# Kernel tuning notes

Measured on AMD Instinct MI355X. Metric: run time of the kernel, lower is better.

Reference implementation:

```python
import jax, jax.numpy as jnp
import numpy as np

N_NODES = 10000
N_EDGES = 160000
NUM_REL = 16
NUM_BLOCKS = 32
BLOCK_SIZE = 4  # input_dim 128 = 32 * 4
INPUT_DIM = NUM_BLOCKS * BLOCK_SIZE


def setup_inputs() -> dict:
    key = jax.random.key(0)
    ks = jax.random.split(key, 6)
    std = float(np.sqrt(2.0) / (2 * BLOCK_SIZE))  # matches reset_parameters
    return {
        "x": jax.random.normal(ks[0], (N_NODES, INPUT_DIM), dtype=jnp.float32),
        "node_keep_mask": jnp.ones((N_NODES,), dtype=bool),
        "source": jax.random.randint(ks[1], (N_EDGES,), 0, N_NODES),
        "target": jax.random.randint(ks[2], (N_EDGES,), 0, N_NODES),
        "edge_type": jax.random.randint(ks[3], (N_EDGES,), 0, NUM_REL),
        "edge_weights": jax.random.uniform(ks[4], (N_EDGES,), dtype=jnp.float32),
        "blocks": jax.random.normal(ks[5], (NUM_REL + 1, NUM_BLOCKS, BLOCK_SIZE, BLOCK_SIZE), dtype=jnp.float32) * std,
    }


def reference(x, node_keep_mask, source, target, edge_type, edge_weights, blocks):
    n = x.shape[0]
    _, nb, bs, _ = blocks.shape
    xb = x.reshape(n, nb, bs)  # (N, B, bs)
    # self-loop transform with last block set; dropped-out nodes stay zero
    self_msg = jnp.einsum('nbi,bij->nbj', xb, blocks[-1])
    out = jnp.where(node_keep_mask[:, None, None], self_msg, 0.0)
    # symmetrize edges: messages flow both directions with same relation/weight
    src2 = jnp.concatenate([source, target])
    tgt2 = jnp.concatenate([target, source])
    et2 = jnp.concatenate([edge_type, edge_type])
    ew2 = jnp.concatenate([edge_weights, edge_weights])
    # per-edge block-diagonal matmul: gather relation blocks then 4x4 block GEMMs
    w_e = blocks[et2]                              # (2E, B, bs, bs)
    m = jnp.einsum('ebi,ebij->ebj', xb[src2], w_e)  # (2E, B, bs)
    m = m * ew2[:, None, None]
    out = out + jax.ops.segment_sum(m, tgt2, num_segments=n)
    return out.reshape(n, nb * bs)
```

## Files before the change

### kernel.cpp

```cpp
#include <hip/hip_runtime.h>

#define INPUT_DIM 128
#define NB 32
#define BS 4
#define CAP 128
#define WSTRIDE_U 12
#define GBLOCKS 1250

typedef _Float16 h2 __attribute__((ext_vector_type(2)));
union HU { unsigned int u; h2 h; };

__device__ inline unsigned int pack_f16(float a, float b) {
    HU v; v.h = h2{(_Float16)a, (_Float16)b}; return v.u;
}
__device__ inline h2 as_h2(unsigned int u) { HU v; v.u = u; return v.h; }

__device__ inline float dot2(h2 a, h2 b, float c) {
    return __builtin_amdgcn_fdot2(a, b, c, false);
}


__global__ void prep_kernel(const float* __restrict__ x, unsigned int* __restrict__ xh,
                            const int* __restrict__ src, const int* __restrict__ tgt,
                            const int* __restrict__ etype, const float* __restrict__ ew,
                            int* __restrict__ counts, int2* __restrict__ msg,
                            int n_edges, int nx8) {
    int i = blockIdx.x * blockDim.x + threadIdx.x;
    if (i < nx8) {
        const float4 a = *(const float4*)(x + (size_t)i * 8);
        const float4 b = *(const float4*)(x + (size_t)i * 8 + 4);
        uint4 o;
        o.x = pack_f16(a.x, a.y);
        o.y = pack_f16(a.z, a.w);
        o.z = pack_f16(b.x, b.y);
        o.w = pack_f16(b.z, b.w);
        *(uint4*)(xh + (size_t)i * 4) = o;
    }
    if (i < n_edges) {
        int s = src[i], t = tgt[i];
        int pk_base = etype[i] << 16;
        int wbits = __float_as_int(ew[i]);
        int pf = atomicAdd(&counts[t], 1);
        msg[t * CAP + pf] = make_int2(s | pk_base, wbits);
        int pb = atomicAdd(&counts[s], 1);
        msg[s * CAP + pb] = make_int2(t | pk_base, wbits);
    }
}

__global__ __launch_bounds__(256, 6)
void gather_kernel(const float* __restrict__ x,
                   const unsigned int* __restrict__ xh,
                   const int* __restrict__ keep,
                   const float* __restrict__ blocks,
                   const int* __restrict__ counts,
                   const int2* __restrict__ msg,
                   float* __restrict__ out, int n_nodes) {
    __shared__ unsigned int Wlds[16 * NB * WSTRIDE_U];

    for (int bi = threadIdx.x; bi < 16 * NB; bi += 256) {
        const float4 r0 = ((const float4*)blocks)[bi * 4 + 0];
        const float4 r1 = ((const float4*)blocks)[bi * 4 + 1];
        const float4 r2 = ((const float4*)blocks)[bi * 4 + 2];
        const float4 r3 = ((const float4*)blocks)[bi * 4 + 3];
        uint4 q0, q1;
        q0.x = pack_f16(r0.x, r1.x); q0.y = pack_f16(r2.x, r3.x);
        q0.z = pack_f16(r0.y, r1.y); q0.w = pack_f16(r2.y, r3.y);
        q1.x = pack_f16(r0.z, r1.z); q1.y = pack_f16(r2.z, r3.z);
        q1.z = pack_f16(r0.w, r1.w); q1.w = pack_f16(r2.w, r3.w);
        *(uint4*)&Wlds[bi * WSTRIDE_U + 0] = q0;
        *(uint4*)&Wlds[bi * WSTRIDE_U + 4] = q1;
    }
    __syncthreads();

    int lane = threadIdx.x & 63;
    int b = lane & 31;
    int slot = lane >> 5;
    int wave_id = (blockIdx.x * blockDim.x + threadIdx.x) >> 6;
    int n_waves = gridDim.x * (blockDim.x >> 6);

    #define DO_MSG(PK, W)                                                     \
        {                                                                     \
            int s_ = (PK) & 0xFFFF;                                           \
            int r_ = (PK) >> 16;                                              \
            const unsigned int* Wp_ = &Wlds[(r_ * NB + b) * WSTRIDE_U];       \
            const uint4 q0 = *(const uint4*)(Wp_ + 0);                        \
            const uint4 q1 = *(const uint4*)(Wp_ + 4);                        \
            const uint2 xp = *(const uint2*)(xh + s_ * 64 + 2 * b);           \
            const h2 xl = as_h2(xp.x), xhh = as_h2(xp.y);                     \
            float m0 = dot2(xl, as_h2(q0.x), dot2(xhh, as_h2(q0.y), 0.f));    \
            float m1 = dot2(xl, as_h2(q0.z), dot2(xhh, as_h2(q0.w), 0.f));    \
            float m2 = dot2(xl, as_h2(q1.x), dot2(xhh, as_h2(q1.y), 0.f));    \
            float m3 = dot2(xl, as_h2(q1.z), dot2(xhh, as_h2(q1.w), 0.f));    \
            acc.x += (W) * m0;                                                \
            acc.y += (W) * m1;                                                \
            acc.z += (W) * m2;                                                \
            acc.w += (W) * m3;                                                \
        }

    for (int n = wave_id; n < n_nodes; n += n_waves) {
        float4 acc = make_float4(0.f, 0.f, 0.f, 0.f);

        if (slot == 0 && keep[n] != 0) {
            const float4 xv = *(const float4*)(x + (size_t)n * INPUT_DIM + b * BS);
            const float* Wp = blocks + (((size_t)16 * NB + b) << 4);
            const float4 c0 = *(const float4*)(Wp + 0);
            const float4 c1 = *(const float4*)(Wp + 4);
            const float4 c2 = *(const float4*)(Wp + 8);
            const float4 c3 = *(const float4*)(Wp + 12);
            acc.x = xv.x * c0.x + xv.y * c1.x + xv.z * c2.x + xv.w * c3.x;
            acc.y = xv.x * c0.y + xv.y * c1.y + xv.z * c2.y + xv.w * c3.y;
            acc.z = xv.x * c0.z + xv.y * c1.z + xv.z * c2.z + xv.w * c3.z;
            acc.w = xv.x * c0.w + xv.y * c1.w + xv.z * c2.w + xv.w * c3.w;
        }

        int cnt = counts[n];
        int base = n * CAP;
        int p = 0;
        for (; p + 8 <= cnt; p += 8) {
            int2 m0 = msg[base + p + 0 + slot];
            int2 m1 = msg[base + p + 2 + slot];
            int2 m2 = msg[base + p + 4 + slot];
            int2 m3 = msg[base + p + 6 + slot];
            float w0 = __int_as_float(m0.y);
            float w1 = __int_as_float(m1.y);
            float w2 = __int_as_float(m2.y);
            float w3 = __int_as_float(m3.y);
            DO_MSG(m0.x, w0);
            DO_MSG(m1.x, w1);
            DO_MSG(m2.x, w2);
            DO_MSG(m3.x, w3);
        }
        for (; p < cnt; p += 2) {
            if (p + slot < cnt) {
                int2 m = msg[base + p + slot];
                DO_MSG(m.x, __int_as_float(m.y));
            }
        }

        acc.x += __shfl_xor(acc.x, 32, 64);
        acc.y += __shfl_xor(acc.y, 32, 64);
        acc.z += __shfl_xor(acc.z, 32, 64);
        acc.w += __shfl_xor(acc.w, 32, 64);

        if (slot == 0)
            *(float4*)(out + (size_t)n * INPUT_DIM + b * BS) = acc;
    }
    #undef DO_MSG
}

extern "C" void kernel_launch(void* const* d_in, const int* in_sizes, int n_in,
                              void* d_out, int out_size, void* d_ws, size_t ws_size,
                              hipStream_t stream) {
    const float* x       = (const float*)d_in[0];
    const int* km        = (const int*)d_in[1];
    const int* source    = (const int*)d_in[2];
    const int* target    = (const int*)d_in[3];
    const int* edge_type = (const int*)d_in[4];
    const float* edge_w  = (const float*)d_in[5];
    const float* blocks  = (const float*)d_in[6];
    float* out           = (float*)d_out;

    int n_nodes = in_sizes[0] / INPUT_DIM;
    int n_edges = in_sizes[2];
    int nx8     = n_nodes * INPUT_DIM / 8;

    int* counts      = (int*)d_ws;
    unsigned int* xh = (unsigned int*)((char*)d_ws + 65536);
    int2* msg        = (int2*)((char*)d_ws + 65536 + (size_t)n_nodes * INPUT_DIM * 2);

    hipMemsetAsync(counts, 0, n_nodes * sizeof(int), stream);
    int prep_threads = (n_edges > nx8) ? n_edges : nx8;
    prep_kernel<<<(prep_threads + 255) / 256, 256, 0, stream>>>(
        x, xh, source, target, edge_type, edge_w, counts, msg, n_edges, nx8);
    gather_kernel<<<GBLOCKS, 256, 0, stream>>>(
        x, xh, km, blocks, counts, msg, out, n_nodes);
}
```

Baseline: 117.0 us.

## Precompute per-relation transformed node features and gather them per edge

The prep kernel now computes x·W_r for every node and all 17 relation block sets, storing the results as fp16 in a large Y table. The gather kernel then only loads one precomputed row per message and accumulates it scaled by the edge weight, replacing the per-edge LDS weight load and dot products. This trades per-edge compute (320k messages) for a dense transform over 17×10000 nodes and a 17-fold larger gather table (~43 MB), which spreads the random gathers over more memory and lowers cache locality. The gather grid is also resized to one wave per node, and prep_threads now covers n_nodes*NB rather than the max of edges and nx8.

```diff
diff --git a/kernel.cpp b/kernel.cpp
--- a/kernel.cpp
+++ b/kernel.cpp
@@ -4,8 +4,7 @@
 #define NB 32
 #define BS 4
 #define CAP 128
-#define WSTRIDE_U 12
-#define GBLOCKS 1250
+#define NREL 17
 
 typedef _Float16 h2 __attribute__((ext_vector_type(2)));
 union HU { unsigned int u; h2 h; };
@@ -15,27 +14,40 @@
 }
 __device__ inline h2 as_h2(unsigned int u) { HU v; v.u = u; return v.h; }
 
-__device__ inline float dot2(h2 a, h2 b, float c) {
-    return __builtin_amdgcn_fdot2(a, b, c, false);
-}
 
+__global__ __launch_bounds__(256)
+void prep_kernel(const float* __restrict__ x, const float* __restrict__ blocks,
+                 const int* __restrict__ src, const int* __restrict__ tgt,
+                 const int* __restrict__ etype, const float* __restrict__ ew,
+                 int* __restrict__ counts, int2* __restrict__ msg,
+                 unsigned int* __restrict__ Y, int n_edges, int n_nodes) {
+    __shared__ float Wlds[NREL * NB * 16];
 
-__global__ void prep_kernel(const float* __restrict__ x, unsigned int* __restrict__ xh,
-                            const int* __restrict__ src, const int* __restrict__ tgt,
-                            const int* __restrict__ etype, const float* __restrict__ ew,
-                            int* __restrict__ counts, int2* __restrict__ msg,
-                            int n_edges, int nx8) {
+    for (int i = threadIdx.x; i < NREL * NB * 4; i += 256)
+        ((float4*)Wlds)[i] = ((const float4*)blocks)[i];
+    __syncthreads();
+
     int i = blockIdx.x * blockDim.x + threadIdx.x;
-    if (i < nx8) {
-        const float4 a = *(const float4*)(x + (size_t)i * 8);
-        const float4 b = *(const float4*)(x + (size_t)i * 8 + 4);
-        uint4 o;
-        o.x = pack_f16(a.x, a.y);
-        o.y = pack_f16(a.z, a.w);
-        o.z = pack_f16(b.x, b.y);
-        o.w = pack_f16(b.z, b.w);
-        *(uint4*)(xh + (size_t)i * 4) = o;
+
+    if (i < n_nodes * NB) {
+        int n = i >> 5;
+        int b = i & 31;
+        const float4 xv = *(const float4*)(x + (size_t)n * INPUT_DIM + b * BS);
+        #pragma unroll
+        for (int r = 0; r < NREL; ++r) {
+            const float4* Wp = (const float4*)&Wlds[(r * NB + b) * 16];
+            const float4 c0 = Wp[0], c1 = Wp[1], c2 = Wp[2], c3 = Wp[3];
+            float y0 = xv.x * c0.x + xv.y * c1.x + xv.z * c2.x + xv.w * c3.x;
+            float y1 = xv.x * c0.y + xv.y * c1.y + xv.z * c2.y + xv.w * c3.y;
+            float y2 = xv.x * c0.z + xv.y * c1.z + xv.z * c2.z + xv.w * c3.z;
+            float y3 = xv.x * c0.w + xv.y * c1.w + xv.z * c2.w + xv.w * c3.w;
+            uint2 o;
+            o.x = pack_f16(y0, y1);
+            o.y = pack_f16(y2, y3);
+            *(uint2*)(Y + (((size_t)(r * n_nodes + n)) << 6) + 2 * b) = o;
+        }
     }
+
     if (i < n_edges) {
         int s = src[i], t = tgt[i];
         int pk_base = etype[i] << 16;
@@ -47,70 +59,42 @@
     }
 }
 
-__global__ __launch_bounds__(256, 6)
-void gather_kernel(const float* __restrict__ x,
-                   const unsigned int* __restrict__ xh,
+__global__ __launch_bounds__(256)
+void gather_kernel(const unsigned int* __restrict__ Y,
                    const int* __restrict__ keep,
-                   const float* __restrict__ blocks,
                    const int* __restrict__ counts,
                    const int2* __restrict__ msg,
                    float* __restrict__ out, int n_nodes) {
-    __shared__ unsigned int Wlds[16 * NB * WSTRIDE_U];
-
-    for (int bi = threadIdx.x; bi < 16 * NB; bi += 256) {
-        const float4 r0 = ((const float4*)blocks)[bi * 4 + 0];
-        const float4 r1 = ((const float4*)blocks)[bi * 4 + 1];
-        const float4 r2 = ((const float4*)blocks)[bi * 4 + 2];
-        const float4 r3 = ((const float4*)blocks)[bi * 4 + 3];
-        uint4 q0, q1;
-        q0.x = pack_f16(r0.x, r1.x); q0.y = pack_f16(r2.x, r3.x);
-        q0.z = pack_f16(r0.y, r1.y); q0.w = pack_f16(r2.y, r3.y);
-        q1.x = pack_f16(r0.z, r1.z); q1.y = pack_f16(r2.z, r3.z);
-        q1.z = pack_f16(r0.w, r1.w); q1.w = pack_f16(r2.w, r3.w);
-        *(uint4*)&Wlds[bi * WSTRIDE_U + 0] = q0;
-        *(uint4*)&Wlds[bi * WSTRIDE_U + 4] = q1;
-    }
-    __syncthreads();
-
     int lane = threadIdx.x & 63;
     int b = lane & 31;
     int slot = lane >> 5;
     int wave_id = (blockIdx.x * blockDim.x + threadIdx.x) >> 6;
     int n_waves = gridDim.x * (blockDim.x >> 6);
 
-    #define DO_MSG(PK, W)                                                     \
-        {                                                                     \
-            int s_ = (PK) & 0xFFFF;                                           \
-            int r_ = (PK) >> 16;                                              \
-            const unsigned int* Wp_ = &Wlds[(r_ * NB + b) * WSTRIDE_U];       \
-            const uint4 q0 = *(const uint4*)(Wp_ + 0);                        \
-            const uint4 q1 = *(const uint4*)(Wp_ + 4);                        \
-            const uint2 xp = *(const uint2*)(xh + s_ * 64 + 2 * b);           \
-            const h2 xl = as_h2(xp.x), xhh = as_h2(xp.y);                     \
-            float m0 = dot2(xl, as_h2(q0.x), dot2(xhh, as_h2(q0.y), 0.f));    \
-            float m1 = dot2(xl, as_h2(q0.z), dot2(xhh, as_h2(q0.w), 0.f));    \
-            float m2 = dot2(xl, as_h2(q1.x), dot2(xhh, as_h2(q1.y), 0.f));    \
-            float m3 = dot2(xl, as_h2(q1.z), dot2(xhh, as_h2(q1.w), 0.f));    \
-            acc.x += (W) * m0;                                                \
-            acc.y += (W) * m1;                                                \
-            acc.z += (W) * m2;                                                \
-            acc.w += (W) * m3;                                                \
+    #define DO_MSG(PK, W)                                                       \
+        {                                                                       \
+            int s_ = (PK) & 0xFFFF;                                             \
+            int r_ = (PK) >> 16;                                                \
+            const uint2 yp = *(const uint2*)(Y +                                \
+                (((size_t)(r_ * n_nodes + s_)) << 6) + 2 * b);                  \
+            const h2 lo = as_h2(yp.x), hi = as_h2(yp.y);                        \
+            acc.x += (W) * (float)lo.x;                                         \
+            acc.y += (W) * (float)lo.y;                                         \
+            acc.z += (W) * (float)hi.x;                                         \
+            acc.w += (W) * (float)hi.y;                                         \
         }
 
     for (int n = wave_id; n < n_nodes; n += n_waves) {
         float4 acc = make_float4(0.f, 0.f, 0.f, 0.f);
 
         if (slot == 0 && keep[n] != 0) {
-            const float4 xv = *(const float4*)(x + (size_t)n * INPUT_DIM + b * BS);
-            const float* Wp = blocks + (((size_t)16 * NB + b) << 4);
-            const float4 c0 = *(const float4*)(Wp + 0);
-            const float4 c1 = *(const float4*)(Wp + 4);
-            const float4 c2 = *(const float4*)(Wp + 8);
-            const float4 c3 = *(const float4*)(Wp + 12);
-            acc.x = xv.x * c0.x + xv.y * c1.x + xv.z * c2.x + xv.w * c3.x;
-            acc.y = xv.x * c0.y + xv.y * c1.y + xv.z * c2.y + xv.w * c3.y;
-            acc.z = xv.x * c0.z + xv.y * c1.z + xv.z * c2.z + xv.w * c3.z;
-            acc.w = xv.x * c0.w + xv.y * c1.w + xv.z * c2.w + xv.w * c3.w;
+            const uint2 yp = *(const uint2*)(Y +
+                (((size_t)(16 * n_nodes + n)) << 6) + 2 * b);
+            const h2 lo = as_h2(yp.x), hi = as_h2(yp.y);
+            acc.x = (float)lo.x;
+            acc.y = (float)lo.y;
+            acc.z = (float)hi.x;
+            acc.w = (float)hi.y;
         }
 
         int cnt = counts[n];
@@ -162,16 +146,20 @@
 
     int n_nodes = in_sizes[0] / INPUT_DIM;
     int n_edges = in_sizes[2];
-    int nx8     = n_nodes * INPUT_DIM / 8;
 
+    size_t msg_bytes = (size_t)n_nodes * CAP * sizeof(int2);
     int* counts      = (int*)d_ws;
-    unsigned int* xh = (unsigned int*)((char*)d_ws + 65536);
-    int2* msg        = (int2*)((char*)d_ws + 65536 + (size_t)n_nodes * INPUT_DIM * 2);
+    int2* msg        = (int2*)((char*)d_ws + 65536);
+    unsigned int* Y  = (unsigned int*)((char*)d_ws + 65536 + msg_bytes);
 
     hipMemsetAsync(counts, 0, n_nodes * sizeof(int), stream);
-    int prep_threads = (n_edges > nx8) ? n_edges : nx8;
+
+    int prep_threads = n_nodes * NB;
     prep_kernel<<<(prep_threads + 255) / 256, 256, 0, stream>>>(
-        x, xh, source, target, edge_type, edge_w, counts, msg, n_edges, nx8);
-    gather_kernel<<<GBLOCKS, 256, 0, stream>>>(
-        x, xh, km, blocks, counts, msg, out, n_nodes);
+        x, blocks, source, target, edge_type, edge_w, counts, msg, Y,
+        n_edges, n_nodes);
+
+    int gather_threads = n_nodes * 64;
+    gather_kernel<<<(gather_threads + 255) / 256, 256, 0, stream>>>(
+        Y, km, counts, msg, out, n_nodes);
 }
```

Result: slower. 121.9 us (+4.2%).
